# Kernel tuning notes

Hardware: AMD Instinct MI355X
Metric: run time of the kernel (lower is better)

The kernel has to match this reference:

```python
import jax, jax.numpy as jnp
import numpy as np

S, E, D, L, K = 32, 64, 256, 5, 5  # sentences, entities, feat dim, labels, support shots


def setup_inputs() -> dict:
    key = jax.random.key(0)
    k1, k2, k3, k4, k5, k6, k7 = jax.random.split(key, 7)
    scale = 1.0 / np.sqrt(D)
    return {
        "sup_entities": jax.random.normal(k1, (L, K, 2 * D), jnp.float32),
        "sup_context": jax.random.normal(k2, (L, K, D), jnp.float32),
        "x": jax.random.normal(k3, (S, E, D), jnp.float32),
        "context": jax.random.normal(k4, (S, E, E, D), jnp.float32),
        "W": jax.random.normal(k5, (D, D), jnp.float32) * scale,
        "Wself": jax.random.normal(k6, (D, D), jnp.float32) * scale,
        "counts": jax.random.randint(k7, (L,), 0, 9, jnp.int32),
    }


def reference(sup_entities, sup_context, x, context, W, Wself, counts):
    # per-label instance-count bias c_n = |n| / (total - |n|)
    cnt = counts.astype(jnp.float32) + 1.0
    total = jnp.sum(cnt)
    c = cnt / (total - cnt)  # [L]

    # prototypes (mean over support instances)
    proto = jnp.mean(sup_entities, axis=1)      # [L, 2D]
    ctx_center = jnp.mean(sup_context, axis=1)  # [L, D]

    # per-label edge weights: 1 / ||context[s,u,v] - ctx_center[k]||^2
    cn2 = jnp.sum(context * context, axis=-1)                        # [S,E,E]
    cc2 = jnp.sum(ctx_center * ctx_center, axis=-1)                  # [L]
    cross = jnp.einsum('suvd,kd->suvk', context, ctx_center)         # [S,E,E,L]
    d2 = cn2[..., None] - 2.0 * cross + cc2                          # [S,E,E,L]
    diag = jnp.eye(E, dtype=bool)
    w = jnp.where(diag[None, :, :, None], 0.0, 1.0 / jnp.maximum(d2, 1e-8))

    # GNN propagation per label: out[s,k,v] = x[s,v]@Wself + sum_u w[s,u,v,k] * (x[s,u]@W)
    xW = x @ W        # [S,E,D]
    xself = x @ Wself  # [S,E,D]
    out = xself[:, None, :, :] + jnp.einsum('suvk,sud->skvd', w, xW)  # [S,L,E,D]

    # squared distance of pred = cat(out[j], out[jp]) to each prototype n
    pa, pb = proto[:, :D], proto[:, D:]  # [L,D] each

    def sqd(o, p):  # o:[S,L,E,D], p:[L,D] -> [S,L,E,L]
        return (jnp.sum(o * o, axis=-1)[..., None]
                - 2.0 * jnp.einsum('skvd,nd->skvn', o, p)
                + jnp.sum(p * p, axis=-1))

    da = sqd(out, pa)  # [S,L,E,L]
    db = sqd(out, pb)  # [S,L,E,L]
    logits = da[:, :, :, None, :] + db[:, :, None, :, :] + c  # [S,L,E,E,L]
    pred = jax.nn.softmax(logits, axis=-1)
    # -> [sentence, entity_j, entity_j', weight_label_k, class_n]
    return jnp.transpose(pred, (0, 2, 3, 1, 4))
```

## Files before the change

### kernel.cpp

```cpp
#include <hip/hip_runtime.h>
#include <hip/hip_bf16.h>

#define SS 32
#define EE 64
#define DD 256
#define LL 5

typedef unsigned int uint32;

static __device__ __forceinline__ ushort f2bf(float f) {
    uint32 u = __float_as_uint(f);
    uint32 r = (u + 0x7FFFu + ((u >> 16) & 1u)) >> 16;
    return (ushort)r;
}
static __device__ __forceinline__ float bf2f(ushort h) {
    return __uint_as_float(((uint32)h) << 16);
}


__global__ __launch_bounds__(256) void k0_setup(
    const float* __restrict__ sup_entities,
    const int*   __restrict__ counts,
    float* __restrict__ ws) {
    int b = blockIdx.x;
    int t = threadIdx.x, lane = t & 63, wv = t >> 6;
    int k = (b >= 5) ? b - 5 : b;
    int off = (b >= 5) ? 256 : 0;
    float s = 0.f;
#pragma unroll
    for (int j = 0; j < 5; j++) s += sup_entities[(k * 5 + j) * 512 + off + t];
    float m = s * 0.2f;
    ws[(b >= 5 ? 1280 : 0) + k * 256 + t] = m;

    __shared__ float part[4];
    float p = m * m;
#pragma unroll
    for (int o = 1; o < 64; o <<= 1) p += __shfl_xor(p, o);
    if (lane == 0) part[wv] = p;
    __syncthreads();
    if (t == 0) ws[2560 + b] = part[0] + part[1] + part[2] + part[3];

    if (b == 0 && t == 0) {
        float cnt[5], tot = 0.f;
#pragma unroll
        for (int q = 0; q < 5; q++) { cnt[q] = (float)counts[q] + 1.0f; tot += cnt[q]; }
#pragma unroll
        for (int q = 0; q < 5; q++) ws[2570 + q] = cnt[q] / (tot - cnt[q]);
    }
}

__global__ __attribute__((amdgpu_waves_per_eu(2, 2))) __launch_bounds__(256)
void k1_gemm(
    const float* __restrict__ x, const float* __restrict__ W,
    const float* __restrict__ Wself, float* __restrict__ ws) {
    float* xself = ws + 4096;
    ushort* xw = (ushort*)(ws + 528384);

    int row0 = blockIdx.x * 8;
    int t = threadIdx.x, lane = t & 63, wv = t >> 6;

    float xreg[8];
    const float* xbase = x + row0 * DD + wv * 64 + lane;
#pragma unroll
    for (int r = 0; r < 8; r++) xreg[r] = xbase[r * DD];

    float4 accW[8], accS[8];
#pragma unroll
    for (int r = 0; r < 8; r++) {
        accW[r] = make_float4(0.f, 0.f, 0.f, 0.f);
        accS[r] = make_float4(0.f, 0.f, 0.f, 0.f);
    }
    const float4* Wp  = ((const float4*)W) + lane;
    const float4* Wsp = ((const float4*)Wself) + lane;
#pragma unroll 2
    for (int i = 0; i < 64; i++) {
        int kk = wv * 64 + i;
        float4 w4  = Wp[kk * 64];
        float4 ws4 = Wsp[kk * 64];
#pragma unroll
        for (int r = 0; r < 8; r++) {
            float xs = __uint_as_float(
                (uint32)__builtin_amdgcn_readlane((int)__float_as_uint(xreg[r]), i));
            accW[r].x = fmaf(xs, w4.x, accW[r].x);
            accW[r].y = fmaf(xs, w4.y, accW[r].y);
            accW[r].z = fmaf(xs, w4.z, accW[r].z);
            accW[r].w = fmaf(xs, w4.w, accW[r].w);
            accS[r].x = fmaf(xs, ws4.x, accS[r].x);
            accS[r].y = fmaf(xs, ws4.y, accS[r].y);
            accS[r].z = fmaf(xs, ws4.z, accS[r].z);
            accS[r].w = fmaf(xs, ws4.w, accS[r].w);
        }
    }
    __shared__ float4 redbuf[4][8][64];
#pragma unroll
    for (int r = 0; r < 8; r++) redbuf[wv][r][lane] = accS[r];
    __syncthreads();
    {
        int r = t >> 5;
#pragma unroll
        for (int f = 0; f < 2; f++) {
            int l4 = (t & 31) + 32 * f;
            float4 a = redbuf[0][r][l4], b = redbuf[1][r][l4];
            float4 c = redbuf[2][r][l4], d = redbuf[3][r][l4];
            float4 s4 = make_float4(a.x + b.x + c.x + d.x, a.y + b.y + c.y + d.y,
                                    a.z + b.z + c.z + d.z, a.w + b.w + c.w + d.w);
            *(float4*)&xself[(row0 + r) * DD + l4 * 4] = s4;
        }
    }
    __syncthreads();
#pragma unroll
    for (int r = 0; r < 8; r++) redbuf[wv][r][lane] = accW[r];
    __syncthreads();
    {
        int r = t >> 5;
#pragma unroll
        for (int f = 0; f < 2; f++) {
            int l4 = (t & 31) + 32 * f;
            float4 a = redbuf[0][r][l4], b = redbuf[1][r][l4];
            float4 c = redbuf[2][r][l4], d = redbuf[3][r][l4];
            float4 s4 = make_float4(a.x + b.x + c.x + d.x, a.y + b.y + c.y + d.y,
                                    a.z + b.z + c.z + d.z, a.w + b.w + c.w + d.w);
            ushort4 h;
            h.x = f2bf(s4.x); h.y = f2bf(s4.y); h.z = f2bf(s4.z); h.w = f2bf(s4.w);
            *(ushort4*)&xw[(row0 + r) * DD + l4 * 4] = h;
        }
    }
}

__global__ __launch_bounds__(256) void k2_w(
    const float* __restrict__ context,
    const float* __restrict__ sup_context,
    float* __restrict__ ws) {
    float* wt = ws + 790528;

    int bx = blockIdx.x;
    int slab = bx >> 1, half = bx & 1;
    int s = slab >> 6, u = slab & 63;
    int t = threadIdx.x, lane = t & 63, wv = t >> 6;
    int g = lane >> 4, gl = lane & 15;
    int G = wv * 4 + g;

    __shared__ float cc_l[1280];
    __shared__ float cc2_l[8];
    __shared__ float wbuf[5][32];

    for (int i = t; i < 1280; i += 256) {
        int k = i >> 8, d = i & 255;
        float sum = 0.f;
#pragma unroll
        for (int j = 0; j < 5; j++) sum += sup_context[(k * 5 + j) * DD + d];
        cc_l[i] = sum * 0.2f;
    }
    __syncthreads();
    if (t < 80) {
        int k = t >> 4, gg = t & 15;
        float p = 0.f;
#pragma unroll
        for (int j = 0; j < 16; j++) { float v = cc_l[k * 256 + gg * 16 + j]; p = fmaf(v, v, p); }
#pragma unroll
        for (int o = 1; o < 16; o <<= 1) p += __shfl_xor(p, o);
        if (gg == 0) cc2_l[k] = p;
    }
    __syncthreads();

    const float* base = context + ((size_t)slab) * (EE * DD) + half * 32 * DD;
    const float* r0p = base + G * DD + gl * 4;
    const float* r1p = base + (16 + G) * DD + gl * 4;

    float cn0 = 0.f, cn1 = 0.f;
    float cr0[5] = {0.f, 0.f, 0.f, 0.f, 0.f};
    float cr1[5] = {0.f, 0.f, 0.f, 0.f, 0.f};
#pragma unroll
    for (int j = 0; j < 4; j++) {
        float4 a = *(const float4*)&r0p[j * 64];
        float4 b = *(const float4*)&r1p[j * 64];
        cn0 = fmaf(a.x, a.x, fmaf(a.y, a.y, fmaf(a.z, a.z, fmaf(a.w, a.w, cn0))));
        cn1 = fmaf(b.x, b.x, fmaf(b.y, b.y, fmaf(b.z, b.z, fmaf(b.w, b.w, cn1))));
#pragma unroll
        for (int k = 0; k < 5; k++) {
            float4 p = *(const float4*)&cc_l[k * 256 + j * 64 + gl * 4];
            cr0[k] = fmaf(a.x, p.x, fmaf(a.y, p.y, fmaf(a.z, p.z, fmaf(a.w, p.w, cr0[k]))));
            cr1[k] = fmaf(b.x, p.x, fmaf(b.y, p.y, fmaf(b.z, p.z, fmaf(b.w, p.w, cr1[k]))));
        }
    }
#pragma unroll
    for (int o = 1; o < 16; o <<= 1) {
        cn0 += __shfl_xor(cn0, o);
        cn1 += __shfl_xor(cn1, o);
#pragma unroll
        for (int k = 0; k < 5; k++) {
            cr0[k] += __shfl_xor(cr0[k], o);
            cr1[k] += __shfl_xor(cr1[k], o);
        }
    }
    if (gl == 0) {
        int v0 = half * 32 + G, v1 = half * 32 + 16 + G;
#pragma unroll
        for (int k = 0; k < 5; k++) {
            float d2a = cn0 - 2.f * cr0[k] + cc2_l[k];
            float d2b = cn1 - 2.f * cr1[k] + cc2_l[k];
            wbuf[k][G]      = (u == v0) ? 0.f : 1.f / fmaxf(d2a, 1e-8f);
            wbuf[k][16 + G] = (u == v1) ? 0.f : 1.f / fmaxf(d2b, 1e-8f);
        }
    }
    __syncthreads();
    if (t < 160) {
        int k = t >> 5, vl = t & 31;
        wt[(((size_t)s * 5 + k) * 64 + u) * 64 + half * 32 + vl] = wbuf[k][vl];
    }
}

__global__ __attribute__((amdgpu_waves_per_eu(2, 2))) __launch_bounds__(256)
void kB(const float* __restrict__ ws) {
    const ushort* xw = (const ushort*)(ws + 528384);
    const float* xself = ws + 4096;
    const float* wt = ws + 790528;
    float* da = (float*)(ws + 1445888);
    float* db = (float*)(ws + 1497088);

    int bx = blockIdx.x;
    int s = bx >> 4, vg = bx & 15;
    int t = threadIdx.x, lane = t & 63, wv = t >> 6;

    __shared__ ushort xw_l[64][256];
    __shared__ float  w_l[5][64][4];

    {
        const uint4* src = (const uint4*)(xw + (size_t)s * (EE * DD));
        uint4* dst = (uint4*)&xw_l[0][0];
#pragma unroll
        for (int j = 0; j < 8; j++) dst[j * 256 + t] = src[j * 256 + t];
    }
    for (int i = t; i < 320; i += 256) {
        int k = i >> 6, u = i & 63;
        *(float4*)&w_l[k][u][0] =
            *(const float4*)&wt[(((size_t)s * 5 + k) * 64 + u) * 64 + vg * 4];
    }
    __syncthreads();

    int v = vg * 4 + wv;
    float4 acc[5];
    {
        float4 xs = *(const float4*)&xself[((size_t)s * 64 + v) * DD + lane * 4];
#pragma unroll
        for (int k = 0; k < 5; k++) acc[k] = xs;
    }

#pragma unroll 4
    for (int u = 0; u < 64; u++) {
        ushort4 h4 = *(const ushort4*)&xw_l[u][lane * 4];
        float4 xv = make_float4(bf2f(h4.x), bf2f(h4.y), bf2f(h4.z), bf2f(h4.w));
#pragma unroll
        for (int k = 0; k < 5; k++) {
            float wk = w_l[k][u][wv];
            acc[k].x = fmaf(wk, xv.x, acc[k].x);
            acc[k].y = fmaf(wk, xv.y, acc[k].y);
            acc[k].z = fmaf(wk, xv.z, acc[k].z);
            acc[k].w = fmaf(wk, xv.w, acc[k].w);
        }
    }

    float4 pA[5], pB[5];
#pragma unroll
    for (int n = 0; n < 5; n++) {
        pA[n] = *(const float4*)&ws[n * 256 + lane * 4];
        pB[n] = *(const float4*)&ws[1280 + n * 256 + lane * 4];
    }
    float pa2r[5], pb2r[5];
#pragma unroll
    for (int n = 0; n < 5; n++) { pa2r[n] = ws[2560 + n]; pb2r[n] = ws[2565 + n]; }

#pragma unroll
    for (int k = 0; k < 5; k++) {
        float4 o = acc[k];
        float r[11];
        r[0] = fmaf(o.x, o.x, fmaf(o.y, o.y, fmaf(o.z, o.z, o.w * o.w)));
#pragma unroll
        for (int n = 0; n < 5; n++) {
            float4 p = pA[n];
            r[1 + n] = fmaf(o.x, p.x, fmaf(o.y, p.y, fmaf(o.z, p.z, o.w * p.w)));
            float4 q = pB[n];
            r[6 + n] = fmaf(o.x, q.x, fmaf(o.y, q.y, fmaf(o.z, q.z, o.w * q.w)));
        }
#pragma unroll
        for (int off = 1; off < 64; off <<= 1) {
#pragma unroll
            for (int q = 0; q < 11; q++) r[q] += __shfl_xor(r[q], off);
        }
        if (lane == 0) {
            size_t idx = (((size_t)s * 5 + k) * 64 + v) * 5;
#pragma unroll
            for (int n = 0; n < 5; n++) {
                da[idx + n] = r[0] - 2.f * r[1 + n] + pa2r[n];
                db[idx + n] = r[0] - 2.f * r[6 + n] + pb2r[n];
            }
        }
    }
}

__global__ __launch_bounds__(320) void kC(const float* __restrict__ ws,
                                          float* __restrict__ out) {
    const float* da = ws + 1445888;
    const float* db = ws + 1497088;
    int bx = blockIdx.x;
    int s = bx >> 6, v1 = bx & 63;
    int t = threadIdx.x;
    int v2 = t / 5, k = t - v2 * 5;

    __shared__ float ob[1600];
    __shared__ float cvs[5];
    if (t < 5) cvs[t] = ws[2570 + t];

    const float* dap = da + (((size_t)s * 5 + k) * 64 + v1) * 5;
    const float* dbp = db + (((size_t)s * 5 + k) * 64 + v2) * 5;
    float l0[5];
#pragma unroll
    for (int n = 0; n < 5; n++) l0[n] = dap[n] + dbp[n];
    __syncthreads();
    float m = -3.4e38f;
#pragma unroll
    for (int n = 0; n < 5; n++) { l0[n] += cvs[n]; m = fmaxf(m, l0[n]); }
    float e[5], sum = 0.f;
#pragma unroll
    for (int n = 0; n < 5; n++) { e[n] = __expf(l0[n] - m); sum += e[n]; }
    float r = 1.f / sum;
#pragma unroll
    for (int n = 0; n < 5; n++) ob[t * 5 + n] = e[n] * r;
    __syncthreads();

    const float4* ob4 = (const float4*)ob;
    float4* op = (float4*)(out + (size_t)bx * 1600);
    for (int i = t; i < 400; i += 320) op[i] = ob4[i];
}

extern "C" void kernel_launch(void* const* d_in, const int* in_sizes, int n_in,
                              void* d_out, int out_size, void* d_ws, size_t ws_size,
                              hipStream_t stream) {
    const float* sup_entities = (const float*)d_in[0];
    const float* sup_context  = (const float*)d_in[1];
    const float* x            = (const float*)d_in[2];
    const float* context      = (const float*)d_in[3];
    const float* W            = (const float*)d_in[4];
    const float* Wself        = (const float*)d_in[5];
    const int*   counts       = (const int*)d_in[6];
    float* out = (float*)d_out;
    float* ws = (float*)d_ws;

    k2_w<<<SS * EE * 2, 256, 0, stream>>>(context, sup_context, ws);
    k1_gemm<<<256, 256, 0, stream>>>(x, W, Wself, ws);
    k0_setup<<<10, 256, 0, stream>>>(sup_entities, counts, ws);
    kB<<<512, 256, 0, stream>>>(ws);
    kC<<<SS * EE, 320, 0, stream>>>(ws, out);
}
```

Measured before the change: 74.67 us.

## Precompute support context centers once and restructure edge-weight kernel with DPP reductions

Moves the per-block recomputation of support context centers and their squared norms out of k2_w into the setup kernel, which now runs first with extra blocks. k2_w processes a whole 64-row slab per block (half as many blocks), keeps center vectors in registers, and replaces shuffle-based 16-lane reductions with DPP row operations. The aim is to remove redundant sup_context reads and reduction work across thousands of blocks. In exchange there is one more serialized dependency at the start and higher register pressure per thread.

```diff
diff --git a/kernel.cpp b/kernel.cpp
--- a/kernel.cpp
+++ b/kernel.cpp
@@ -17,35 +17,63 @@
     return __uint_as_float(((uint32)h) << 16);
 }
 
+template <int CTRL>
+static __device__ __forceinline__ float dpp_add(float x) {
+    int y = __builtin_amdgcn_update_dpp(0, __float_as_int(x), CTRL, 0xF, 0xF, true);
+    return x + __int_as_float(y);
+}
+static __device__ __forceinline__ float red16(float x) {
+    x = dpp_add<0xB1>(x);
+    x = dpp_add<0x4E>(x);
+    x = dpp_add<0x141>(x);
+    x = dpp_add<0x140>(x);
+    return x;
+}
+
 
 __global__ __launch_bounds__(256) void k0_setup(
     const float* __restrict__ sup_entities,
+    const float* __restrict__ sup_context,
     const int*   __restrict__ counts,
     float* __restrict__ ws) {
     int b = blockIdx.x;
     int t = threadIdx.x, lane = t & 63, wv = t >> 6;
-    int k = (b >= 5) ? b - 5 : b;
-    int off = (b >= 5) ? 256 : 0;
-    float s = 0.f;
-#pragma unroll
-    for (int j = 0; j < 5; j++) s += sup_entities[(k * 5 + j) * 512 + off + t];
-    float m = s * 0.2f;
-    ws[(b >= 5 ? 1280 : 0) + k * 256 + t] = m;
-
     __shared__ float part[4];
-    float p = m * m;
-#pragma unroll
-    for (int o = 1; o < 64; o <<= 1) p += __shfl_xor(p, o);
-    if (lane == 0) part[wv] = p;
-    __syncthreads();
-    if (t == 0) ws[2560 + b] = part[0] + part[1] + part[2] + part[3];
-
-    if (b == 0 && t == 0) {
-        float cnt[5], tot = 0.f;
-#pragma unroll
-        for (int q = 0; q < 5; q++) { cnt[q] = (float)counts[q] + 1.0f; tot += cnt[q]; }
-#pragma unroll
-        for (int q = 0; q < 5; q++) ws[2570 + q] = cnt[q] / (tot - cnt[q]);
+
+    if (b < 10) {
+        int k = (b >= 5) ? b - 5 : b;
+        int off = (b >= 5) ? 256 : 0;
+        float s = 0.f;
+#pragma unroll
+        for (int j = 0; j < 5; j++) s += sup_entities[(k * 5 + j) * 512 + off + t];
+        float m = s * 0.2f;
+        ws[(b >= 5 ? 1280 : 0) + k * 256 + t] = m;
+        float p = m * m;
+#pragma unroll
+        for (int o = 1; o < 64; o <<= 1) p += __shfl_xor(p, o);
+        if (lane == 0) part[wv] = p;
+        __syncthreads();
+        if (t == 0) ws[2560 + b] = part[0] + part[1] + part[2] + part[3];
+    } else {
+        int k = b - 10;
+        float s = 0.f;
+#pragma unroll
+        for (int j = 0; j < 5; j++) s += sup_context[(k * 5 + j) * DD + t];
+        float m = s * 0.2f;
+        ws[2576 + k * 256 + t] = m;
+        float p = m * m;
+#pragma unroll
+        for (int o = 1; o < 64; o <<= 1) p += __shfl_xor(p, o);
+        if (lane == 0) part[wv] = p;
+        __syncthreads();
+        if (t == 0) ws[3856 + k] = part[0] + part[1] + part[2] + part[3];
+        if (b == 10 && t == 1) {
+            float cnt[5], tot = 0.f;
+#pragma unroll
+            for (int q = 0; q < 5; q++) { cnt[q] = (float)counts[q] + 1.0f; tot += cnt[q]; }
+#pragma unroll
+            for (int q = 0; q < 5; q++) ws[2570 + q] = cnt[q] / (tot - cnt[q]);
+        }
     }
 }
 
@@ -127,86 +155,71 @@
     }
 }
 
-__global__ __launch_bounds__(256) void k2_w(
-    const float* __restrict__ context,
-    const float* __restrict__ sup_context,
-    float* __restrict__ ws) {
+__global__ __attribute__((amdgpu_waves_per_eu(4, 4))) __launch_bounds__(256)
+void k2_w(const float* __restrict__ context, float* __restrict__ ws) {
     float* wt = ws + 790528;
 
     int bx = blockIdx.x;
-    int slab = bx >> 1, half = bx & 1;
-    int s = slab >> 6, u = slab & 63;
+    int s = bx >> 6, u = bx & 63;
     int t = threadIdx.x, lane = t & 63, wv = t >> 6;
     int g = lane >> 4, gl = lane & 15;
     int G = wv * 4 + g;
 
     __shared__ float cc_l[1280];
     __shared__ float cc2_l[8];
-    __shared__ float wbuf[5][32];
-
-    for (int i = t; i < 1280; i += 256) {
-        int k = i >> 8, d = i & 255;
-        float sum = 0.f;
-#pragma unroll
-        for (int j = 0; j < 5; j++) sum += sup_context[(k * 5 + j) * DD + d];
-        cc_l[i] = sum * 0.2f;
-    }
-    __syncthreads();
-    if (t < 80) {
-        int k = t >> 4, gg = t & 15;
-        float p = 0.f;
-#pragma unroll
-        for (int j = 0; j < 16; j++) { float v = cc_l[k * 256 + gg * 16 + j]; p = fmaf(v, v, p); }
-#pragma unroll
-        for (int o = 1; o < 16; o <<= 1) p += __shfl_xor(p, o);
-        if (gg == 0) cc2_l[k] = p;
-    }
-    __syncthreads();
-
-    const float* base = context + ((size_t)slab) * (EE * DD) + half * 32 * DD;
-    const float* r0p = base + G * DD + gl * 4;
-    const float* r1p = base + (16 + G) * DD + gl * 4;
-
-    float cn0 = 0.f, cn1 = 0.f;
-    float cr0[5] = {0.f, 0.f, 0.f, 0.f, 0.f};
-    float cr1[5] = {0.f, 0.f, 0.f, 0.f, 0.f};
-#pragma unroll
-    for (int j = 0; j < 4; j++) {
-        float4 a = *(const float4*)&r0p[j * 64];
-        float4 b = *(const float4*)&r1p[j * 64];
-        cn0 = fmaf(a.x, a.x, fmaf(a.y, a.y, fmaf(a.z, a.z, fmaf(a.w, a.w, cn0))));
-        cn1 = fmaf(b.x, b.x, fmaf(b.y, b.y, fmaf(b.z, b.z, fmaf(b.w, b.w, cn1))));
-#pragma unroll
-        for (int k = 0; k < 5; k++) {
-            float4 p = *(const float4*)&cc_l[k * 256 + j * 64 + gl * 4];
-            cr0[k] = fmaf(a.x, p.x, fmaf(a.y, p.y, fmaf(a.z, p.z, fmaf(a.w, p.w, cr0[k]))));
-            cr1[k] = fmaf(b.x, p.x, fmaf(b.y, p.y, fmaf(b.z, p.z, fmaf(b.w, p.w, cr1[k]))));
-        }
-    }
-#pragma unroll
-    for (int o = 1; o < 16; o <<= 1) {
-        cn0 += __shfl_xor(cn0, o);
-        cn1 += __shfl_xor(cn1, o);
-#pragma unroll
-        for (int k = 0; k < 5; k++) {
-            cr0[k] += __shfl_xor(cr0[k], o);
-            cr1[k] += __shfl_xor(cr1[k], o);
-        }
-    }
-    if (gl == 0) {
-        int v0 = half * 32 + G, v1 = half * 32 + 16 + G;
-#pragma unroll
-        for (int k = 0; k < 5; k++) {
-            float d2a = cn0 - 2.f * cr0[k] + cc2_l[k];
-            float d2b = cn1 - 2.f * cr1[k] + cc2_l[k];
-            wbuf[k][G]      = (u == v0) ? 0.f : 1.f / fmaxf(d2a, 1e-8f);
-            wbuf[k][16 + G] = (u == v1) ? 0.f : 1.f / fmaxf(d2b, 1e-8f);
-        }
-    }
-    __syncthreads();
-    if (t < 160) {
-        int k = t >> 5, vl = t & 31;
-        wt[(((size_t)s * 5 + k) * 64 + u) * 64 + half * 32 + vl] = wbuf[k][vl];
+    __shared__ float wbuf[5][64];
+
+    for (int i = t; i < 320; i += 256)
+        ((float4*)cc_l)[i] = ((const float4*)(ws + 2576))[i];
+    if (t < 5) cc2_l[t] = ws[3856 + t];
+    __syncthreads();
+
+    float4 cc[5][4];
+    float cc2r[5];
+#pragma unroll
+    for (int k = 0; k < 5; k++) {
+#pragma unroll
+        for (int j = 0; j < 4; j++)
+            cc[k][j] = *(const float4*)&cc_l[k * 256 + j * 64 + gl * 4];
+        cc2r[k] = cc2_l[k];
+    }
+
+    const float* base = context + (size_t)bx * (EE * DD) + gl * 4;
+#pragma unroll
+    for (int p = 0; p < 4; p++) {
+        int v = p * 16 + G;
+        const float* row = base + v * DD;
+        float4 a[4];
+#pragma unroll
+        for (int j = 0; j < 4; j++) a[j] = *(const float4*)&row[j * 64];
+
+        float cn = 0.f;
+        float cr[5] = {0.f, 0.f, 0.f, 0.f, 0.f};
+#pragma unroll
+        for (int j = 0; j < 4; j++) {
+            float4 c4 = a[j];
+            cn = fmaf(c4.x, c4.x, fmaf(c4.y, c4.y, fmaf(c4.z, c4.z, fmaf(c4.w, c4.w, cn))));
+#pragma unroll
+            for (int k = 0; k < 5; k++) {
+                float4 pp = cc[k][j];
+                cr[k] = fmaf(c4.x, pp.x, fmaf(c4.y, pp.y, fmaf(c4.z, pp.z, fmaf(c4.w, pp.w, cr[k]))));
+            }
+        }
+        cn = red16(cn);
+#pragma unroll
+        for (int k = 0; k < 5; k++) cr[k] = red16(cr[k]);
+        if (gl == 0) {
+#pragma unroll
+            for (int k = 0; k < 5; k++) {
+                float d2 = cn - 2.f * cr[k] + cc2r[k];
+                wbuf[k][v] = (u == v) ? 0.f : 1.f / fmaxf(d2, 1e-8f);
+            }
+        }
+    }
+    __syncthreads();
+    for (int i = t; i < 320; i += 256) {
+        int k = i >> 6, v = i & 63;
+        wt[(((size_t)s * 5 + k) * 64 + u) * 64 + v] = wbuf[k][v];
     }
 }
 
@@ -346,9 +359,9 @@
     float* out = (float*)d_out;
     float* ws = (float*)d_ws;
 
-    k2_w<<<SS * EE * 2, 256, 0, stream>>>(context, sup_context, ws);
+    k0_setup<<<15, 256, 0, stream>>>(sup_entities, sup_context, counts, ws);
+    k2_w<<<SS * EE, 256, 0, stream>>>(context, ws);
     k1_gemm<<<256, 256, 0, stream>>>(x, W, Wself, ws);
-    k0_setup<<<10, 256, 0, stream>>>(sup_entities, counts, ws);
     kB<<<512, 256, 0, stream>>>(ws);
     kC<<<SS * EE, 320, 0, stream>>>(ws, out);
 }
```

Result: faster. 73.09 us (-2.1%).
